# Performance work log

Measured on AMD Instinct MI355X. Metric: run time of the kernel, lower is better.

Reference implementation:

```python
import jax, jax.numpy as jnp
import numpy as np

B, MAXN, NVT, NINP, NHID, NHEAD, NL, NZ = 1024, 32, 16, 256, 512, 8, 6, 64
HID = MAXN * NHID
EPS = 1e-5
SCALE = 1.0 / np.sqrt(NHID // NHEAD)


def setup_inputs() -> dict:
    key = jax.random.key(0)
    ks = jax.random.split(key, 16)
    s = 0.02
    d = {}
    d["node_types"] = jax.random.randint(ks[0], (B, MAXN), 0, NVT, dtype=jnp.int32)
    d["adj_bits"] = jax.random.randint(ks[1], (B, MAXN, MAXN), 0, 2, dtype=jnp.int32)
    d["Wpos"] = jax.random.normal(ks[2], (MAXN, NINP), jnp.float32) * s
    d["bpos"] = jnp.zeros((NINP,), jnp.float32)
    d["Wnode"] = jax.random.normal(ks[3], (NVT, NINP), jnp.float32) * s
    d["bnode"] = jnp.zeros((NINP,), jnp.float32)
    for i, n in enumerate(["Wq", "Wk", "Wv", "Wo", "W1", "W2"]):
        d["enc_" + n] = jax.random.normal(ks[4 + i], (NL, NHID, NHID), jnp.float32) * s
    for n in ["bq", "bk", "bv", "bo", "b1", "b2"]:
        d["enc_" + n] = jnp.zeros((NL, NHID), jnp.float32)
    d["ln1_g"] = jnp.ones((NL, NHID), jnp.float32)
    d["ln1_b"] = jnp.zeros((NL, NHID), jnp.float32)
    d["ln2_g"] = jnp.ones((NL, NHID), jnp.float32)
    d["ln2_b"] = jnp.zeros((NL, NHID), jnp.float32)
    d["Wfc1"] = jax.random.normal(ks[10], (HID, NZ), jnp.float32) * s
    d["bfc1"] = jnp.zeros((NZ,), jnp.float32)
    d["Wfc2"] = jax.random.normal(ks[11], (HID, NZ), jnp.float32) * s
    d["bfc2"] = jnp.zeros((NZ,), jnp.float32)
    return d


def _ln(x, g, b):
    m = x.mean(-1, keepdims=True)
    v = ((x - m) ** 2).mean(-1, keepdims=True)
    return (x - m) * jax.lax.rsqrt(v + EPS) * g + b


def _dag_attn_bias(adj_bits):
    # _mask_generate: transitive closure via matmul powers; log-depth squaring
    # over a boolean semiring (min(.,1) after each add) gives identical reachability.
    iu = jnp.triu(jnp.ones((MAXN, MAXN), jnp.float32), 1)  # enforce DAG
    adj = adj_bits.astype(jnp.float32) * iu  # [B,N,N]
    reach = adj
    for _ in range(int(np.ceil(np.log2(MAXN)))):
        reach = jnp.minimum(reach + jnp.matmul(reach, reach), 1.0)
    # original: mask = (sum_powers + I) < 0.5 (True=disallowed), then transpose(1,2)
    allowed = (jnp.swapaxes(reach, 1, 2) + jnp.eye(MAXN, dtype=jnp.float32)) > 0.5
    return jnp.where(allowed, 0.0, -jnp.inf)[:, None, :, :]  # [B,1,N,N]


def _encode(node_types, adj_bits, Wpos, bpos, Wnode, bnode,
            enc_Wq, enc_bq, enc_Wk, enc_bk, enc_Wv, enc_bv, enc_Wo, enc_bo,
            ln1_g, ln1_b, enc_W1, enc_b1, enc_W2, enc_b2, ln2_g, ln2_b,
            Wfc1, bfc1, Wfc2, bfc2):
    node_feat = jax.nn.relu(Wnode[node_types] + bnode)               # [B,N,ninp]
    pos_feat = jnp.broadcast_to(Wpos + bpos, (B, MAXN, NINP))        # position = node index
    x = jnp.concatenate([node_feat, pos_feat], -1)                   # [B,N,512]
    bias = _dag_attn_bias(adj_bits)
    dh = NHID // NHEAD
    for l in range(NL):
        q = (x @ enc_Wq[l] + enc_bq[l]).reshape(B, MAXN, NHEAD, dh)
        k = (x @ enc_Wk[l] + enc_bk[l]).reshape(B, MAXN, NHEAD, dh)
        v = (x @ enc_Wv[l] + enc_bv[l]).reshape(B, MAXN, NHEAD, dh)
        s = jnp.einsum('bqhd,bkhd->bhqk', q, k) * SCALE + bias
        a = jax.nn.softmax(s, axis=-1)
        o = jnp.einsum('bhqk,bkhd->bqhd', a, v).reshape(B, MAXN, NHID)
        x = _ln(x + o @ enc_Wo[l] + enc_bo[l], ln1_g[l], ln1_b[l])    # post-LN
        f = jax.nn.relu(x @ enc_W1[l] + enc_b1[l]) @ enc_W2[l] + enc_b2[l]
        x = _ln(x + f, ln2_g[l], ln2_b[l])
    mem = x.reshape(B, HID)
    return mem @ Wfc1 + bfc1, mem @ Wfc2 + bfc2


def reference(node_types, adj_bits, Wpos, bpos, Wnode, bnode,
              enc_Wq, enc_bq, enc_Wk, enc_bk, enc_Wv, enc_bv, enc_Wo, enc_bo,
              ln1_g, ln1_b, enc_W1, enc_b1, enc_W2, enc_b2, ln2_g, ln2_b,
              Wfc1, bfc1, Wfc2, bfc2):
    return _encode(node_types, adj_bits, Wpos, bpos, Wnode, bnode,
                   enc_Wq, enc_bq, enc_Wk, enc_bk, enc_Wv, enc_bv, enc_Wo, enc_bo,
                   ln1_g, ln1_b, enc_W1, enc_b1, enc_W2, enc_b2, ln2_g, ln2_b,
                   Wfc1, bfc1, Wfc2, bfc2)
```

## Files before the change

kernel.cpp:

```cpp
#include <hip/hip_runtime.h>


typedef unsigned short u16;
typedef unsigned int u32;
typedef __attribute__((ext_vector_type(8))) short bf16x8;
typedef __attribute__((ext_vector_type(4))) float f32x4;

#define NB 1024
#define MAXN 32
#define NHID 512
#define NHEAD 8
#define NLAY 6
#define MTOT (NB * MAXN)
#define ATT_SCALE 0.125f
#define LN_EPS 1e-5f

__device__ __forceinline__ float bf2f(u16 h) { return __uint_as_float(((u32)h) << 16); }
__device__ __forceinline__ u16 f2bf(float f) {
  u32 u = __float_as_uint(f);
  return (u16)((u + 0x7fffu + ((u >> 16) & 1u)) >> 16);
}

__device__ __forceinline__ void gload16(const void* g, void* l) {
  __builtin_amdgcn_global_load_lds((const __attribute__((address_space(1))) void*)g,
                                   (__attribute__((address_space(3))) void*)l, 16, 0, 0);
}

__device__ __forceinline__ void xcd_remap(int l, int NX, int& mt, int& nt) {
  int xcd = l & 7;
  int s = l >> 3;
  int mg = s / NX;
  nt = s - mg * NX;
  mt = mg * 8 + xcd;
}

__global__ __launch_bounds__(256) void mask_k(const int* __restrict__ adj, u32* __restrict__ mask) {
  __shared__ u32 r[8][32];
  int tid = threadIdx.x;
  int g = tid >> 5, i = tid & 31;
  int b = blockIdx.x * 8 + g;
  const int* ab = adj + ((long)b * 32 + i) * 32;
  u32 m = 0;
  for (int j = i + 1; j < 32; ++j)
    if (ab[j]) m |= (1u << j);
  r[g][i] = m;
  __syncthreads();
  for (int it = 0; it < 5; ++it) {
    u32 cur = r[g][i];
    u32 acc = cur;
    #pragma unroll
    for (int j = 0; j < 32; ++j)
      if ((cur >> j) & 1u) acc |= r[g][j];
    __syncthreads();
    r[g][i] = acc;
    __syncthreads();
  }
  u32 am = 1u << i;
  #pragma unroll
  for (int k = 0; k < 32; ++k) am |= ((r[g][k] >> i) & 1u) << k;
  mask[b * 32 + i] = am;
}

__global__ __launch_bounds__(256) void embed_k(const int* __restrict__ types,
    const float* __restrict__ Wpos, const float* __restrict__ bpos,
    const float* __restrict__ Wnode, const float* __restrict__ bnode,
    u16* __restrict__ xb) {
  int i = blockIdx.x * 256 + threadIdx.x;
  int row = i >> 7, c = (i & 127) * 4;
  int b = row >> 5, n = row & 31;
  float v[4];
  if (c < 256) {
    int tp = types[b * 32 + n];
    const float* w = &Wnode[tp * 256 + c];
    #pragma unroll
    for (int j = 0; j < 4; ++j) v[j] = fmaxf(w[j] + bnode[c + j], 0.f);
  } else {
    int cc = c - 256;
    const float* w = &Wpos[n * 256 + cc];
    #pragma unroll
    for (int j = 0; j < 4; ++j) v[j] = w[j] + bpos[cc + j];
  }
  ushort4 h; h.x = f2bf(v[0]); h.y = f2bf(v[1]); h.z = f2bf(v[2]); h.w = f2bf(v[3]);
  *(ushort4*)&xb[(long)row * NHID + c] = h;
}

__global__ __launch_bounds__(256) void tconv_k(const float* __restrict__ W,
    u16* __restrict__ Wt, int n_off, int n_total) {
  __shared__ float tile[32][33];
  int l = blockIdx.z;
  int k0 = blockIdx.x * 32, n0 = blockIdx.y * 32;
  int tx = threadIdx.x & 31, ty = threadIdx.x >> 5;
  const float* src = W + (size_t)l * NHID * NHID;
  #pragma unroll
  for (int i = 0; i < 4; ++i)
    tile[ty + 8 * i][tx] = src[(size_t)(k0 + ty + 8 * i) * NHID + n0 + tx];
  __syncthreads();
  u16* dst = Wt + (size_t)l * n_total * NHID;
  #pragma unroll
  for (int i = 0; i < 4; ++i)
    dst[(size_t)(n_off + n0 + ty + 8 * i) * NHID + k0 + tx] = f2bf(tile[tx][ty + 8 * i]);
}

__global__ __launch_bounds__(256, 4) void gemm_qkv(
    const u16* __restrict__ A, const u16* __restrict__ Bt,
    const float* __restrict__ bq, const float* __restrict__ bk,
    const float* __restrict__ bv, u16* __restrict__ qk, u16* __restrict__ v) {
  __shared__ u16 As[2][128 * 32];
  __shared__ u16 Bs[2][128 * 32];
  const int tid = threadIdx.x;
  const int wave = tid >> 6, lane = tid & 63;
  int mt, nt_;
  xcd_remap(blockIdx.x + gridDim.x * blockIdx.y, gridDim.x, mt, nt_);
  const long m0 = (long)mt * 128;
  const int n0 = nt_ * 128;
  const int wr = wave >> 1, wc = wave & 1;
  const int srow = lane >> 2;
  const int sg = (lane & 3) ^ ((srow >> 1) & 3);
  const int fr = lane & 15;
  const int kq = lane >> 4;
  f32x4 acc[4][4] = {};

  auto stage = [&](int buf, int k0) {
    #pragma unroll
    for (int i = 0; i < 2; ++i) {
      int c = 2 * wave + i;
      gload16(A + (m0 + 16 * c + srow) * 512L + k0 + sg * 8, &As[buf][c * 512]);
      gload16(Bt + (long)(n0 + 16 * c + srow) * 512 + k0 + sg * 8, &Bs[buf][c * 512]);
    }
  };
  stage(0, 0);
  const int kqx = (kq ^ ((fr >> 1) & 3)) * 8;
  #pragma unroll 1
  for (int t = 0; t < 16; ++t) {
    asm volatile("s_waitcnt vmcnt(0)" ::: "memory");
    __builtin_amdgcn_s_barrier();
    if (t + 1 < 16) stage((t + 1) & 1, (t + 1) * 32);
    const u16* Asl = As[t & 1];
    const u16* Bsl = Bs[t & 1];
    __builtin_amdgcn_s_setprio(1);
    bf16x8 af[4], bfv[4];
    #pragma unroll
    for (int mi = 0; mi < 4; ++mi)
      af[mi] = *(const bf16x8*)&Asl[(wr * 64 + mi * 16 + fr) * 32 + kqx];
    #pragma unroll
    for (int ni = 0; ni < 4; ++ni)
      bfv[ni] = *(const bf16x8*)&Bsl[(wc * 64 + ni * 16 + fr) * 32 + kqx];
    #pragma unroll
    for (int mi = 0; mi < 4; ++mi)
      #pragma unroll
      for (int ni = 0; ni < 4; ++ni)
        acc[mi][ni] = __builtin_amdgcn_mfma_f32_16x16x32_bf16(bfv[ni], af[mi], acc[mi][ni], 0, 0, 0);
    __builtin_amdgcn_s_setprio(0);
  }

  #pragma unroll
  for (int mi = 0; mi < 4; ++mi) {
    long r = m0 + wr * 64 + mi * 16 + fr;
    #pragma unroll
    for (int ni = 0; ni < 4; ++ni) {
      int n = n0 + wc * 64 + ni * 16 + kq * 4;
      const float* bp = (n < 512) ? bq : ((n < 1024) ? bk : bv);
      float4 bvv = *(const float4*)&bp[n & 511];
      ushort4 st;
      st.x = f2bf(acc[mi][ni][0] + bvv.x);
      st.y = f2bf(acc[mi][ni][1] + bvv.y);
      st.z = f2bf(acc[mi][ni][2] + bvv.z);
      st.w = f2bf(acc[mi][ni][3] + bvv.w);
      if (n < 1024) *(ushort4*)&qk[r * 1024 + n] = st;
      else          *(ushort4*)&v[r * 512 + (n - 1024)] = st;
    }
  }
}

__global__ __launch_bounds__(256, 4) void gemm_relu(
    const u16* __restrict__ A, const u16* __restrict__ Bt,
    const float* __restrict__ bias0, u16* __restrict__ Cout) {
  __shared__ u16 As[2][128 * 32];
  __shared__ u16 Bs[2][128 * 32];
  const int tid = threadIdx.x;
  const int wave = tid >> 6, lane = tid & 63;
  int mt, nt_;
  xcd_remap(blockIdx.x + gridDim.x * blockIdx.y, gridDim.x, mt, nt_);
  const long m0 = (long)mt * 128;
  const int n0 = nt_ * 128;
  const int wr = wave >> 1, wc = wave & 1;
  const int srow = lane >> 2;
  const int sg = (lane & 3) ^ ((srow >> 1) & 3);
  const int fr = lane & 15;
  const int kq = lane >> 4;
  f32x4 acc[4][4] = {};

  auto stage = [&](int buf, int k0) {
    #pragma unroll
    for (int i = 0; i < 2; ++i) {
      int c = 2 * wave + i;
      gload16(A + (m0 + 16 * c + srow) * 512L + k0 + sg * 8, &As[buf][c * 512]);
      gload16(Bt + (long)(n0 + 16 * c + srow) * 512 + k0 + sg * 8, &Bs[buf][c * 512]);
    }
  };
  stage(0, 0);
  const int kqx = (kq ^ ((fr >> 1) & 3)) * 8;
  #pragma unroll 1
  for (int t = 0; t < 16; ++t) {
    asm volatile("s_waitcnt vmcnt(0)" ::: "memory");
    __builtin_amdgcn_s_barrier();
    if (t + 1 < 16) stage((t + 1) & 1, (t + 1) * 32);
    const u16* Asl = As[t & 1];
    const u16* Bsl = Bs[t & 1];
    __builtin_amdgcn_s_setprio(1);
    bf16x8 af[4], bfv[4];
    #pragma unroll
    for (int mi = 0; mi < 4; ++mi)
      af[mi] = *(const bf16x8*)&Asl[(wr * 64 + mi * 16 + fr) * 32 + kqx];
    #pragma unroll
    for (int ni = 0; ni < 4; ++ni)
      bfv[ni] = *(const bf16x8*)&Bsl[(wc * 64 + ni * 16 + fr) * 32 + kqx];
    #pragma unroll
    for (int mi = 0; mi < 4; ++mi)
      #pragma unroll
      for (int ni = 0; ni < 4; ++ni)
        acc[mi][ni] = __builtin_amdgcn_mfma_f32_16x16x32_bf16(bfv[ni], af[mi], acc[mi][ni], 0, 0, 0);
    __builtin_amdgcn_s_setprio(0);
  }

  #pragma unroll
  for (int mi = 0; mi < 4; ++mi) {
    long r = m0 + wr * 64 + mi * 16 + fr;
    #pragma unroll
    for (int ni = 0; ni < 4; ++ni) {
      int n = n0 + wc * 64 + ni * 16 + kq * 4;
      float4 bvv = *(const float4*)&bias0[n];
      ushort4 st;
      st.x = f2bf(fmaxf(acc[mi][ni][0] + bvv.x, 0.f));
      st.y = f2bf(fmaxf(acc[mi][ni][1] + bvv.y, 0.f));
      st.z = f2bf(fmaxf(acc[mi][ni][2] + bvv.z, 0.f));
      st.w = f2bf(fmaxf(acc[mi][ni][3] + bvv.w, 0.f));
      *(ushort4*)&Cout[r * 512 + n] = st;
    }
  }
}

__global__ __launch_bounds__(512, 2) void gemm_ln(
    const u16* __restrict__ A, const u16* __restrict__ Bt,
    const float* __restrict__ bias0, const float* __restrict__ g,
    const float* __restrict__ b, u16* __restrict__ xb) {
  __shared__ u16 As[2][128 * 32];
  __shared__ u16 Bs[2][512 * 32];
  const int tid = threadIdx.x;
  const int wave = tid >> 6, lane = tid & 63;
  const long m0 = (long)blockIdx.x * 128;
  const int wr = wave >> 2, wc = wave & 3;
  const int srow = lane >> 2;
  const int sg = (lane & 3) ^ ((srow >> 1) & 3);
  const int fr = lane & 15;
  const int kq = lane >> 4;
  f32x4 acc[4][8] = {};

  auto stage = [&](int buf, int k0) {
    gload16(A + (m0 + 16 * wave + srow) * 512L + k0 + sg * 8, &As[buf][wave * 512]);
    #pragma unroll
    for (int i = 0; i < 4; ++i) {
      int c = 4 * wave + i;
      gload16(Bt + (long)(16 * c + srow) * 512 + k0 + sg * 8, &Bs[buf][c * 512]);
    }
  };
  stage(0, 0);
  const int kqx = (kq ^ ((fr >> 1) & 3)) * 8;
  #pragma unroll 1
  for (int t = 0; t < 16; ++t) {
    asm volatile("s_waitcnt vmcnt(0)" ::: "memory");
    __builtin_amdgcn_s_barrier();
    if (t + 1 < 16) stage((t + 1) & 1, (t + 1) * 32);
    const u16* Asl = As[t & 1];
    const u16* Bsl = Bs[t & 1];
    __builtin_amdgcn_s_setprio(1);
    bf16x8 af[4], bfv[8];
    #pragma unroll
    for (int mi = 0; mi < 4; ++mi)
      af[mi] = *(const bf16x8*)&Asl[(wr * 64 + mi * 16 + fr) * 32 + kqx];
    #pragma unroll
    for (int ni = 0; ni < 8; ++ni)
      bfv[ni] = *(const bf16x8*)&Bsl[(wc * 128 + ni * 16 + fr) * 32 + kqx];
    #pragma unroll
    for (int mi = 0; mi < 4; ++mi)
      #pragma unroll
      for (int ni = 0; ni < 8; ++ni)
        acc[mi][ni] = __builtin_amdgcn_mfma_f32_16x16x32_bf16(bfv[ni], af[mi], acc[mi][ni], 0, 0, 0);
    __builtin_amdgcn_s_setprio(0);
  }

  float s[4], sq[4];
  #pragma unroll
  for (int mi = 0; mi < 4; ++mi) {
    long r = m0 + wr * 64 + mi * 16 + fr;
    float ss = 0.f, qq = 0.f;
    #pragma unroll
    for (int ni = 0; ni < 8; ++ni) {
      int n = wc * 128 + ni * 16 + kq * 4;
      float4 bvv = *(const float4*)&bias0[n];
      ushort4 rv = *(const ushort4*)&xb[r * 512 + n];
      float y0 = acc[mi][ni][0] + bvv.x + bf2f(rv.x);
      float y1 = acc[mi][ni][1] + bvv.y + bf2f(rv.y);
      float y2 = acc[mi][ni][2] + bvv.z + bf2f(rv.z);
      float y3 = acc[mi][ni][3] + bvv.w + bf2f(rv.w);
      acc[mi][ni][0] = y0; acc[mi][ni][1] = y1;
      acc[mi][ni][2] = y2; acc[mi][ni][3] = y3;
      ss += y0 + y1 + y2 + y3;
      qq += y0 * y0 + y1 * y1 + y2 * y2 + y3 * y3;
    }
    s[mi] = ss; sq[mi] = qq;
  }
  #pragma unroll
  for (int mi = 0; mi < 4; ++mi) {
    s[mi] += __shfl_xor(s[mi], 16);  sq[mi] += __shfl_xor(sq[mi], 16);
    s[mi] += __shfl_xor(s[mi], 32);  sq[mi] += __shfl_xor(sq[mi], 32);
  }
  __syncthreads();
  float* red = (float*)&As[0][0];
  if (lane < 16) {
    #pragma unroll
    for (int mi = 0; mi < 4; ++mi) {
      int idx = ((wr * 64 + mi * 16 + fr) * 4 + wc) * 2;
      red[idx] = s[mi];
      red[idx + 1] = sq[mi];
    }
  }
  __syncthreads();
  #pragma unroll
  for (int mi = 0; mi < 4; ++mi) {
    int rl = wr * 64 + mi * 16 + fr;
    float S = red[(rl * 4 + 0) * 2] + red[(rl * 4 + 1) * 2] + red[(rl * 4 + 2) * 2] + red[(rl * 4 + 3) * 2];
    float Q = red[(rl * 4 + 0) * 2 + 1] + red[(rl * 4 + 1) * 2 + 1] + red[(rl * 4 + 2) * 2 + 1] + red[(rl * 4 + 3) * 2 + 1];
    float mean = S * (1.f / 512.f);
    float inv = rsqrtf(Q * (1.f / 512.f) - mean * mean + LN_EPS);
    long r = m0 + rl;
    #pragma unroll
    for (int ni = 0; ni < 8; ++ni) {
      int n = wc * 128 + ni * 16 + kq * 4;
      float4 g4 = *(const float4*)&g[n];
      float4 b4 = *(const float4*)&b[n];
      ushort4 st;
      st.x = f2bf((acc[mi][ni][0] - mean) * inv * g4.x + b4.x);
      st.y = f2bf((acc[mi][ni][1] - mean) * inv * g4.y + b4.y);
      st.z = f2bf((acc[mi][ni][2] - mean) * inv * g4.z + b4.z);
      st.w = f2bf((acc[mi][ni][3] - mean) * inv * g4.w + b4.w);
      *(ushort4*)&xb[r * 512 + n] = st;
    }
  }
}

__global__ __launch_bounds__(256) void attn_k(const u16* __restrict__ qk,
    const u16* __restrict__ vfull, const u32* __restrict__ mask, u16* __restrict__ o) {
  __shared__ u16 vs_[4][64][40];
  __shared__ u16 p_lds[4][32][40];
  int tid = threadIdx.x;
  int w = tid >> 6, lane = tid & 63;
  int idx = blockIdx.x * 4 + w;
  int b = idx >> 3, h = idx & 7;
  const u16* qbase = qk + (long)b * 32 * 1024 + h * 64;
  const u16* kbase = qbase + 512;
  int g = lane >> 4, r = lane & 15;

  int node = lane >> 1, dh = lane & 1;
  const u16* vsrc = vfull + ((long)b * 32 + node) * 512 + h * 64 + dh * 32;
  bf16x8 vr[4];
  #pragma unroll
  for (int i = 0; i < 4; ++i) vr[i] = *(const bf16x8*)(vsrc + i * 8);

  f32x4 s[2][2] = {};
  #pragma unroll
  for (int ks = 0; ks < 2; ++ks) {
    bf16x8 kf[2], qf[2];
    #pragma unroll
    for (int mi = 0; mi < 2; ++mi)
      kf[mi] = *(const bf16x8*)(kbase + (long)(mi * 16 + r) * 1024 + ks * 32 + g * 8);
    #pragma unroll
    for (int nj = 0; nj < 2; ++nj)
      qf[nj] = *(const bf16x8*)(qbase + (long)(nj * 16 + r) * 1024 + ks * 32 + g * 8);
    #pragma unroll
    for (int mi = 0; mi < 2; ++mi)
      #pragma unroll
      for (int nj = 0; nj < 2; ++nj)
        s[mi][nj] = __builtin_amdgcn_mfma_f32_16x16x32_bf16(kf[mi], qf[nj], s[mi][nj], 0, 0, 0);
  }

  #pragma unroll
  for (int i = 0; i < 4; ++i)
    #pragma unroll
    for (int t = 0; t < 8; ++t)
      vs_[w][dh * 32 + i * 8 + t][node] = (u16)vr[i][t];

  #pragma unroll
  for (int nj = 0; nj < 2; ++nj) {
    int q = nj * 16 + r;
    u32 mk = mask[b * 32 + q];
    float vv[8];
    float mx = -1e30f;
    #pragma unroll
    for (int mi = 0; mi < 2; ++mi)
      #pragma unroll
      for (int j = 0; j < 4; ++j) {
        int k = mi * 16 + g * 4 + j;
        float val = ((mk >> k) & 1u) ? s[mi][nj][j] * ATT_SCALE : -1e30f;
        vv[mi * 4 + j] = val;
        mx = fmaxf(mx, val);
      }
    mx = fmaxf(mx, __shfl_xor(mx, 16));
    mx = fmaxf(mx, __shfl_xor(mx, 32));
    float sum = 0.f;
    #pragma unroll
    for (int i = 0; i < 8; ++i) { vv[i] = __expf(vv[i] - mx); sum += vv[i]; }
    sum += __shfl_xor(sum, 16);
    sum += __shfl_xor(sum, 32);
    float inv = 1.f / sum;
    #pragma unroll
    for (int mi = 0; mi < 2; ++mi) {
      ushort4 pk;
      pk.x = f2bf(vv[mi * 4 + 0] * inv);
      pk.y = f2bf(vv[mi * 4 + 1] * inv);
      pk.z = f2bf(vv[mi * 4 + 2] * inv);
      pk.w = f2bf(vv[mi * 4 + 3] * inv);
      *(ushort4*)&p_lds[w][q][mi * 16 + g * 4] = pk;
    }
  }

  bf16x8 pa[2];
  #pragma unroll
  for (int mi = 0; mi < 2; ++mi)
    pa[mi] = *(const bf16x8*)&p_lds[w][mi * 16 + r][g * 8];
  f32x4 oacc[2][4] = {};
  #pragma unroll
  for (int nd = 0; nd < 4; ++nd) {
    bf16x8 vf = *(const bf16x8*)&vs_[w][nd * 16 + r][g * 8];
    #pragma unroll
    for (int mi = 0; mi < 2; ++mi)
      oacc[mi][nd] = __builtin_amdgcn_mfma_f32_16x16x32_bf16(pa[mi], vf, oacc[mi][nd], 0, 0, 0);
  }
  #pragma unroll
  for (int mi = 0; mi < 2; ++mi)
    #pragma unroll
    for (int j = 0; j < 4; ++j) {
      int q = mi * 16 + g * 4 + j;
      u16* og = o + ((long)b * 32 + q) * NHID + h * 64;
      #pragma unroll
      for (int nd = 0; nd < 4; ++nd)
        og[nd * 16 + r] = f2bf(oacc[mi][nd][j]);
    }
}

__global__ __launch_bounds__(256) void fcT_k(const float* __restrict__ W1,
    const float* __restrict__ W2, u16* __restrict__ Wt) {
  __shared__ float t[64][65];
  int sel = blockIdx.y;
  const float* W = sel ? W2 : W1;
  int k0 = blockIdx.x * 64;
  int tx = threadIdx.x & 63, ty = threadIdx.x >> 6;
  #pragma unroll
  for (int i = 0; i < 16; ++i)
    t[ty + 4 * i][tx] = W[(long)(k0 + ty + 4 * i) * 64 + tx];
  __syncthreads();
  #pragma unroll
  for (int i = 0; i < 16; ++i)
    Wt[(long)(sel * 64 + ty + 4 * i) * 16384 + k0 + tx] = f2bf(t[tx][ty + 4 * i]);
}

__global__ __launch_bounds__(256, 4) void gemm_fc(const u16* __restrict__ A,
    const u16* __restrict__ Bt, float* __restrict__ part) {
  __shared__ u16 As[2][128 * 32];
  __shared__ u16 Bs[2][128 * 32];
  const int tid = threadIdx.x;
  const int wave = tid >> 6, lane = tid & 63;
  const int ks = blockIdx.x;
  const long m0 = (long)blockIdx.y * 128;
  const int kbase = ks * 512;
  const int wr = wave >> 1, wc = wave & 1;
  const int srow = lane >> 2;
  const int sg = (lane & 3) ^ ((srow >> 1) & 3);
  const int fr = lane & 15;
  const int kq = lane >> 4;
  f32x4 acc[4][4] = {};
  auto stage = [&](int buf, int k0) {
    #pragma unroll
    for (int i = 0; i < 2; ++i) {
      int c = 2 * wave + i;
      gload16(A + (m0 + 16 * c + srow) * 16384L + kbase + k0 + sg * 8, &As[buf][c * 512]);
      gload16(Bt + (long)(16 * c + srow) * 16384L + kbase + k0 + sg * 8, &Bs[buf][c * 512]);
    }
  };
  stage(0, 0);
  const int kqx = (kq ^ ((fr >> 1) & 3)) * 8;
  #pragma unroll 1
  for (int t = 0; t < 16; ++t) {
    asm volatile("s_waitcnt vmcnt(0)" ::: "memory");
    __builtin_amdgcn_s_barrier();
    if (t + 1 < 16) stage((t + 1) & 1, (t + 1) * 32);
    const u16* Asl = As[t & 1];
    const u16* Bsl = Bs[t & 1];
    __builtin_amdgcn_s_setprio(1);
    bf16x8 af[4], bfv[4];
    #pragma unroll
    for (int mi = 0; mi < 4; ++mi)
      af[mi] = *(const bf16x8*)&Asl[(wr * 64 + mi * 16 + fr) * 32 + kqx];
    #pragma unroll
    for (int ni = 0; ni < 4; ++ni)
      bfv[ni] = *(const bf16x8*)&Bsl[(wc * 64 + ni * 16 + fr) * 32 + kqx];
    #pragma unroll
    for (int mi = 0; mi < 4; ++mi)
      #pragma unroll
      for (int ni = 0; ni < 4; ++ni)
        acc[mi][ni] = __builtin_amdgcn_mfma_f32_16x16x32_bf16(bfv[ni], af[mi], acc[mi][ni], 0, 0, 0);
    __builtin_amdgcn_s_setprio(0);
  }
  #pragma unroll
  for (int mi = 0; mi < 4; ++mi) {
    long rr = m0 + wr * 64 + mi * 16 + fr;
    #pragma unroll
    for (int ni = 0; ni < 4; ++ni) {
      int n = wc * 64 + ni * 16 + kq * 4;
      *(float4*)&part[((long)ks * 1024 + rr) * 128 + n] =
          make_float4(acc[mi][ni][0], acc[mi][ni][1], acc[mi][ni][2], acc[mi][ni][3]);
    }
  }
}

__global__ __launch_bounds__(256) void fc_red_k(const float* __restrict__ part,
    const float* __restrict__ bfc1, const float* __restrict__ bfc2,
    float* __restrict__ out) {
  int idx = blockIdx.x * 256 + threadIdx.x;
  int sel = idx >> 16;
  int rem = idx & 65535;
  int b = rem >> 6, z = rem & 63;
  float v = sel ? bfc2[z] : bfc1[z];
  #pragma unroll
  for (int ks = 0; ks < 32; ++ks)
    v += part[((long)ks * 1024 + b) * 128 + sel * 64 + z];
  out[idx] = v;
}

extern "C" void kernel_launch(void* const* d_in, const int* in_sizes, int n_in,
                              void* d_out, int out_size, void* d_ws, size_t ws_size,
                              hipStream_t stream) {
  const int* node_types = (const int*)d_in[0];
  const int* adj_bits = (const int*)d_in[1];
  const float* Wpos = (const float*)d_in[2];
  const float* bpos = (const float*)d_in[3];
  const float* Wnode = (const float*)d_in[4];
  const float* bnode = (const float*)d_in[5];
  const float* eWq = (const float*)d_in[6];
  const float* eWk = (const float*)d_in[7];
  const float* eWv = (const float*)d_in[8];
  const float* eWo = (const float*)d_in[9];
  const float* eW1 = (const float*)d_in[10];
  const float* eW2 = (const float*)d_in[11];
  const float* ebq = (const float*)d_in[12];
  const float* ebk = (const float*)d_in[13];
  const float* ebv = (const float*)d_in[14];
  const float* ebo = (const float*)d_in[15];
  const float* eb1 = (const float*)d_in[16];
  const float* eb2 = (const float*)d_in[17];
  const float* ln1g = (const float*)d_in[18];
  const float* ln1b = (const float*)d_in[19];
  const float* ln2g = (const float*)d_in[20];
  const float* ln2b = (const float*)d_in[21];
  const float* Wfc1 = (const float*)d_in[22];
  const float* bfc1 = (const float*)d_in[23];
  const float* Wfc2 = (const float*)d_in[24];
  const float* bfc2 = (const float*)d_in[25];

  char* ws = (char*)d_ws;
  size_t off = 0;
  auto carve = [&](size_t bytes) {
    void* p = ws + off;
    off += (bytes + 255) & ~(size_t)255;
    return p;
  };
  u16* Wqkv_t = (u16*)carve((size_t)NLAY * 1536 * 512 * 2);
  u16* Wo_t = (u16*)carve((size_t)NLAY * 512 * 512 * 2);
  u16* W1_t = (u16*)carve((size_t)NLAY * 512 * 512 * 2);
  u16* W2_t = (u16*)carve((size_t)NLAY * 512 * 512 * 2);
  u16* xb = (u16*)carve((size_t)MTOT * NHID * 2);
  u16* qk = (u16*)carve((size_t)MTOT * 1024 * 2);
  u16* vbuf = (u16*)carve((size_t)MTOT * NHID * 2);
  u16* obuf = (u16*)carve((size_t)MTOT * NHID * 2);
  u32* maskb = (u32*)carve((size_t)NB * MAXN * 4);
  u16* hbuf = obuf;
  u16* Wt_fc = qk;
  float* part_fc = (float*)obuf;

  mask_k<<<NB / 8, 256, 0, stream>>>(adj_bits, maskb);
  embed_k<<<(MTOT * 128) / 256, 256, 0, stream>>>(node_types, Wpos, bpos, Wnode, bnode, xb);
  dim3 tg(16, 16, NLAY);
  tconv_k<<<tg, 256, 0, stream>>>(eWq, Wqkv_t, 0, 1536);
  tconv_k<<<tg, 256, 0, stream>>>(eWk, Wqkv_t, 512, 1536);
  tconv_k<<<tg, 256, 0, stream>>>(eWv, Wqkv_t, 1024, 1536);
  tconv_k<<<tg, 256, 0, stream>>>(eWo, Wo_t, 0, 512);
  tconv_k<<<tg, 256, 0, stream>>>(eW1, W1_t, 0, 512);
  tconv_k<<<tg, 256, 0, stream>>>(eW2, W2_t, 0, 512);

  for (int l = 0; l < NLAY; ++l) {
    size_t lw = (size_t)l * 512 * 512;
    gemm_qkv<<<dim3(12, MTOT / 128), 256, 0, stream>>>(
        xb, Wqkv_t + (size_t)l * 1536 * 512,
        ebq + l * 512, ebk + l * 512, ebv + l * 512, qk, vbuf);
    attn_k<<<NB * NHEAD / 4, 256, 0, stream>>>(qk, vbuf, maskb, obuf);
    gemm_ln<<<MTOT / 128, 512, 0, stream>>>(
        obuf, Wo_t + lw, ebo + l * 512, ln1g + l * 512, ln1b + l * 512, xb);
    gemm_relu<<<dim3(4, MTOT / 128), 256, 0, stream>>>(
        xb, W1_t + lw, eb1 + l * 512, hbuf);
    gemm_ln<<<MTOT / 128, 512, 0, stream>>>(
        hbuf, W2_t + lw, eb2 + l * 512, ln2g + l * 512, ln2b + l * 512, xb);
  }

  fcT_k<<<dim3(256, 2), 256, 0, stream>>>(Wfc1, Wfc2, Wt_fc);
  gemm_fc<<<dim3(32, 8), 256, 0, stream>>>(xb, Wt_fc, part_fc);
  fc_red_k<<<512, 256, 0, stream>>>(part_fc, bfc1, bfc2, (float*)d_out);
}
```

Before: 1.313 ms.

## Enlarge QKV GEMM to 256x256 tiles with 8 waves and phased K-pipeline

The fused QKV projection GEMM moves from 128x128 tiles with 4 waves and K-step 32 to 256x256 tiles with 8 waves and K-step 64. Loads for the next K-tile are split into four quarter-stages interleaved with four compute phases, and the LDS swizzle becomes XOR-8. This raises arithmetic intensity per tile and overlaps global loads with MFMA work, at the cost of more LDS (128KB), more accumulator registers and fewer blocks (768) for the GPU to schedule.

```diff
diff --git a/kernel.cpp b/kernel.cpp
--- a/kernel.cpp
+++ b/kernel.cpp
@@ -101,64 +101,92 @@
     dst[(size_t)(n_off + n0 + ty + 8 * i) * NHID + k0 + tx] = f2bf(tile[tx][ty + 8 * i]);
 }
 
-__global__ __launch_bounds__(256, 4) void gemm_qkv(
+__global__ __launch_bounds__(512, 2) void gemm_qkv(
     const u16* __restrict__ A, const u16* __restrict__ Bt,
     const float* __restrict__ bq, const float* __restrict__ bk,
     const float* __restrict__ bv, u16* __restrict__ qk, u16* __restrict__ v) {
-  __shared__ u16 As[2][128 * 32];
-  __shared__ u16 Bs[2][128 * 32];
+  __shared__ u16 Al[2][2][128 * 64];
+  __shared__ u16 Bl[2][2][128 * 64];
   const int tid = threadIdx.x;
-  const int wave = tid >> 6, lane = tid & 63;
+  const int lane = tid & 63;
+  const int wave = tid >> 6;
   int mt, nt_;
   xcd_remap(blockIdx.x + gridDim.x * blockIdx.y, gridDim.x, mt, nt_);
-  const long m0 = (long)mt * 128;
-  const int n0 = nt_ * 128;
-  const int wr = wave >> 1, wc = wave & 1;
-  const int srow = lane >> 2;
-  const int sg = (lane & 3) ^ ((srow >> 1) & 3);
-  const int fr = lane & 15;
-  const int kq = lane >> 4;
-  f32x4 acc[4][4] = {};
-
-  auto stage = [&](int buf, int k0) {
-    #pragma unroll
-    for (int i = 0; i < 2; ++i) {
-      int c = 2 * wave + i;
-      gload16(A + (m0 + 16 * c + srow) * 512L + k0 + sg * 8, &As[buf][c * 512]);
-      gload16(Bt + (long)(n0 + 16 * c + srow) * 512 + k0 + sg * 8, &Bs[buf][c * 512]);
+  const long m0 = (long)mt * 256;
+  const int n0 = nt_ * 256;
+  const int wr = wave >> 2;
+  const int wcn = wave & 3;
+  const int fr = lane & 15, kq = lane >> 4;
+  const int sr = tid >> 3, sp = tid & 7;
+  const int sgg = sp ^ (sr & 7);
+  f32x4 acc[8][4] = {};
+
+  auto stageH = [&](int kt, int hsel) {
+    int buf = kt & 1;
+    int kof = kt * 64 + sgg * 8;
+    if (hsel < 2) {
+      const u16* src = A + (m0 + hsel * 128 + sr) * 512L + kof;
+      u16* dst = &Al[buf][hsel][sr * 64 + sp * 8];
+      gload16(src, dst);
+      gload16(src + 64 * 512L, dst + 64 * 64);
+    } else {
+      const u16* src = Bt + (long)(n0 + (hsel - 2) * 128 + sr) * 512 + kof;
+      u16* dst = &Bl[buf][hsel - 2][sr * 64 + sp * 8];
+      gload16(src, dst);
+      gload16(src + 64 * 512L, dst + 64 * 64);
     }
   };
-  stage(0, 0);
-  const int kqx = (kq ^ ((fr >> 1) & 3)) * 8;
+  stageH(0, 0); stageH(0, 1); stageH(0, 2); stageH(0, 3);
+
   #pragma unroll 1
-  for (int t = 0; t < 16; ++t) {
-    asm volatile("s_waitcnt vmcnt(0)" ::: "memory");
-    __builtin_amdgcn_s_barrier();
-    if (t + 1 < 16) stage((t + 1) & 1, (t + 1) * 32);
-    const u16* Asl = As[t & 1];
-    const u16* Bsl = Bs[t & 1];
-    __builtin_amdgcn_s_setprio(1);
-    bf16x8 af[4], bfv[4];
-    #pragma unroll
-    for (int mi = 0; mi < 4; ++mi)
-      af[mi] = *(const bf16x8*)&Asl[(wr * 64 + mi * 16 + fr) * 32 + kqx];
-    #pragma unroll
-    for (int ni = 0; ni < 4; ++ni)
-      bfv[ni] = *(const bf16x8*)&Bsl[(wc * 64 + ni * 16 + fr) * 32 + kqx];
-    #pragma unroll
-    for (int mi = 0; mi < 4; ++mi)
-      #pragma unroll
-      for (int ni = 0; ni < 4; ++ni)
-        acc[mi][ni] = __builtin_amdgcn_mfma_f32_16x16x32_bf16(bfv[ni], af[mi], acc[mi][ni], 0, 0, 0);
-    __builtin_amdgcn_s_setprio(0);
-  }
-
-  #pragma unroll
-  for (int mi = 0; mi < 4; ++mi) {
-    long r = m0 + wr * 64 + mi * 16 + fr;
+  for (int kt = 0; kt < 8; ++kt) {
+    const int buf = kt & 1;
+    const u16* Ah = &Al[buf][wr][0];
+    #pragma unroll
+    for (int ph = 0; ph < 4; ++ph) {
+      if (kt < 7) stageH(kt + 1, ph);
+      if (ph == 0) {
+        if (kt < 7) asm volatile("s_waitcnt vmcnt(2)" ::: "memory");
+        else        asm volatile("s_waitcnt vmcnt(0)" ::: "memory");
+        __builtin_amdgcn_s_barrier();
+      }
+      const int mih = ph >> 1, nih = ph & 1;
+      bf16x8 af[4][2], bfv[2][2];
+      #pragma unroll
+      for (int kh = 0; kh < 2; ++kh) {
+        #pragma unroll
+        for (int m2 = 0; m2 < 4; ++m2) {
+          int r = mih * 64 + m2 * 16 + fr;
+          int p = (kh * 4 + kq) ^ (r & 7);
+          af[m2][kh] = *(const bf16x8*)&Ah[r * 64 + p * 8];
+        }
+        #pragma unroll
+        for (int n2 = 0; n2 < 2; ++n2) {
+          int c = wcn * 64 + nih * 32 + n2 * 16 + fr;
+          int p = (kh * 4 + kq) ^ (c & 7);
+          bfv[n2][kh] = *(const bf16x8*)&Bl[buf][c >> 7][(c & 127) * 64 + p * 8];
+        }
+      }
+      __builtin_amdgcn_s_setprio(1);
+      #pragma unroll
+      for (int kh = 0; kh < 2; ++kh)
+        #pragma unroll
+        for (int m2 = 0; m2 < 4; ++m2)
+          #pragma unroll
+          for (int n2 = 0; n2 < 2; ++n2)
+            acc[mih * 4 + m2][nih * 2 + n2] = __builtin_amdgcn_mfma_f32_16x16x32_bf16(
+                bfv[n2][kh], af[m2][kh], acc[mih * 4 + m2][nih * 2 + n2], 0, 0, 0);
+      __builtin_amdgcn_s_setprio(0);
+      if (ph == 3) __builtin_amdgcn_s_barrier();
+    }
+  }
+
+  #pragma unroll
+  for (int mi = 0; mi < 8; ++mi) {
+    long r = m0 + wr * 128 + mi * 16 + fr;
     #pragma unroll
     for (int ni = 0; ni < 4; ++ni) {
-      int n = n0 + wc * 64 + ni * 16 + kq * 4;
+      int n = n0 + wcn * 64 + ni * 16 + kq * 4;
       const float* bp = (n < 512) ? bq : ((n < 1024) ? bk : bv);
       float4 bvv = *(const float4*)&bp[n & 511];
       ushort4 st;
@@ -599,7 +627,7 @@
 
   for (int l = 0; l < NLAY; ++l) {
     size_t lw = (size_t)l * 512 * 512;
-    gemm_qkv<<<dim3(12, MTOT / 128), 256, 0, stream>>>(
+    gemm_qkv<<<dim3(6, MTOT / 256), 512, 0, stream>>>(
         xb, Wqkv_t + (size_t)l * 1536 * 512,
         ebq + l * 512, ebk + l * 512, ebv + l * 512, qk, vbuf);
     attn_k<<<NB * NHEAD / 4, 256, 0, stream>>>(qk, vbuf, maskb, obuf);
```

New measurement: 1.348 ms. 1.03x slower.
